# Kernel tuning notes

Hardware: AMD Instinct MI355X
Metric: run time of the kernel (lower is better)

Reference implementation:

```python
import jax, jax.numpy as jnp
import numpy as np

# Spike nonlinearity with straight-through surrogate gradient
# fwd: z = (v_scaled > 0); bwd: dz/dv = clamp(1 - |v_scaled|, min=0)
@jax.custom_vjp
def spike(v_scaled):
    return (v_scaled > 0).astype(v_scaled.dtype)

def _spike_fwd(v_scaled):
    return spike(v_scaled), v_scaled

def _spike_bwd(v_scaled, g):
    return (g * jnp.maximum(1.0 - jnp.abs(v_scaled), 0.0),)

spike.defvjp(_spike_fwd, _spike_bwd)

_H = np.array([-0.00285825, 0.09859432, 0.07954306, 0.08560576, 0.0910411, 0.10557652,
               0.04608637, 0.07096123, 0.01989892, 0.03412642, 0.03321506, 0.01300904,
               -0.02348068, 0.06102338, -0.00509757, 0.00051896], dtype=np.float32)
_D = np.array([0.04908372, -0.00948576, 0.00083943, 0.07961489, 0.08128168, 0.02395899,
               0.05197346, 0.01595683, 0.02185501, 0.01893722, 0.0074682, -0.00088913,
               0.01660369, 0.00298292, 0.0071363, 0.00279426], dtype=np.float32)
_T = np.array([0.20153396, -0.01304637, -0.19541621, 0.19903184, 0.1529713, -0.00479887,
               0.07102165, 0.02109929, 0.01368383, -0.00360851, -0.01454873, -0.03991705,
               -0.00440092, -0.06122432, -0.02989412, -0.04975629], dtype=np.float32)


def setup_inputs() -> dict:
    key = jax.random.key(0)
    x = jax.random.normal(key, (64, 1024, 1024), dtype=jnp.float32)
    return {
        "x": x,
        "h": jnp.asarray(_H),
        "d": jnp.asarray(_D),
        "T": jnp.asarray(_T),
    }


def reference(x, h, d, T):
    signs = jax.lax.stop_gradient(jnp.sign(x))  # detached in original
    x_abs = jnp.abs(x)

    def step(carry, hdT):
        v, z, out = carry
        ht, dt, Tt = hdT
        v = v - z * ht
        v_scaled = (v - Tt) / (jnp.abs(v) + 1.0)
        z = spike(v_scaled)
        out = out + z * dt
        return (v, z, out), None

    init = (x_abs, jnp.zeros_like(x_abs), jnp.zeros_like(x_abs))
    (_, _, out), _ = jax.lax.scan(step, init, (h, d, T))  # K=16 steps
    return out * signs
```

## Files before the change

kernel.cpp:

```cpp
#include <hip/hip_runtime.h>


#define BIN_B0 0x3D800000u
#define BIN_B1 0x3FC00000u
#define BIN_RANGE 0x02400000u
#define NBIN 4096
#define BIN_STEP 9216u
#define NSIDE_MAX 512
#define SCANTAG 0xFFC00000u

#define W_NSIDE 0
#define W_LO 1
#define W_HI 2
#define W_LUT 4
#define W_SIDE (W_LUT + NBIN)
#define WS_WORDS (W_SIDE + 4 * NSIDE_MAX)

__device__ __forceinline__ int predmask16(float a, const float* __restrict__ hh,
                                          const float* __restrict__ TT) {
    float v = a, z = 0.0f;
    int m = 0;
#pragma unroll
    for (int k = 0; k < 16; ++k) {
        v = fmaf(-z, hh[k], v);
        int zb = (v > TT[k]) ? 1 : 0;
        z = zb ? 1.0f : 0.0f;
        m |= zb << k;
    }
    return m;
}

__device__ __forceinline__ unsigned int valbits(int m, const float* __restrict__ dd) {
    float acc = 0.0f;
#pragma unroll
    for (int k = 0; k < 16; ++k)
        acc = ((m >> k) & 1) ? (acc + dd[k]) : acc;
    return __float_as_uint(acc);
}

__device__ __forceinline__ float scan_exact(unsigned int ab, const float* __restrict__ hh,
                                            const float* __restrict__ dd,
                                            const float* __restrict__ TT) {
    float v = __uint_as_float(ab), z = 0.0f, acc = 0.0f;
#pragma unroll
    for (int k = 0; k < 16; ++k) {
        v = fmaf(-z, hh[k], v);
        z = (v > TT[k]) ? 1.0f : 0.0f;
        acc = fmaf(z, dd[k], acc);
    }
    return acc;
}

__global__ __launch_bounds__(256) void snn_build(
    const float* __restrict__ h, const float* __restrict__ d,
    const float* __restrict__ T, unsigned int* __restrict__ ws) {
    const int u = blockIdx.x * 256 + threadIdx.x;
    if (u >= NBIN + 2) return;
    float hh[16], dd[16], TT[16];
#pragma unroll
    for (int k = 0; k < 16; ++k) { hh[k] = h[k]; dd[k] = d[k]; TT[k] = T[k]; }

    if (u == NBIN) {
        int mA = predmask16(__uint_as_float(0u), hh, TT);
        int mB = predmask16(__uint_as_float(BIN_B0 - 1u), hh, TT);
        ws[W_LO] = (mA == mB) ? valbits(mA, dd) : SCANTAG;
        return;
    }
    if (u == NBIN + 1) {
        int mA = predmask16(__uint_as_float(BIN_B1), hh, TT);
        int mB = predmask16(__uint_as_float(0x7F7FFFFFu), hh, TT);
        ws[W_HI] = (mA == mB) ? valbits(mA, dd) : SCANTAG;
        return;
    }

    const unsigned int Lb = BIN_B0 + (unsigned int)u * BIN_STEP;
    const unsigned int Hb = Lb + (BIN_STEP - 1u);
    const int mL = predmask16(__uint_as_float(Lb), hh, TT);
    const int mH = predmask16(__uint_as_float(Hb), hh, TT);
    if (mL == mH) { ws[W_LUT + u] = valbits(mL, dd); return; }

    unsigned int lo = Lb, hi = Hb;
    int mhi = mH;
    while (hi - lo > 1u) {
        unsigned int mid = lo + ((hi - lo) >> 1);
        int mm = predmask16(__uint_as_float(mid), hh, TT);
        if (mm == mL) lo = mid; else { hi = mid; mhi = mm; }
    }
    const unsigned int p1 = hi;
    const int m1 = mhi;

    unsigned int p2 = 0u;
    int m2 = m1;
    bool two = false, ok = true;
    if (m1 != mH) {
        lo = p1; hi = Hb; mhi = mH;
        while (hi - lo > 1u) {
            unsigned int mid = lo + ((hi - lo) >> 1);
            int mm = predmask16(__uint_as_float(mid), hh, TT);
            if (mm == m1) lo = mid; else { hi = mid; mhi = mm; }
        }
        p2 = hi;
        m2 = mhi;
        two = true;
        ok = (m2 == mH);
    }
    if (ok) {
        int idx = atomicAdd((int*)&ws[W_NSIDE], 1);
        if (idx < NSIDE_MAX) {
            const unsigned int o1 = p1 - Lb;
            const unsigned int o2 = two ? (p2 - Lb) : 0xFFFFu;
            ws[W_SIDE + 4 * idx + 0] = (o2 << 16) | o1;
            ws[W_SIDE + 4 * idx + 1] = valbits(mL, dd);
            ws[W_SIDE + 4 * idx + 2] = valbits(m1, dd);
            ws[W_SIDE + 4 * idx + 3] = valbits(m2, dd);
            ws[W_LUT + u] = 0x7F800000u | (unsigned int)idx;
        } else {
            ws[W_LUT + u] = SCANTAG;
        }
    } else {
        ws[W_LUT + u] = SCANTAG;
    }
}

__device__ __forceinline__ float lut_elem(float xe,
                                          const unsigned int* __restrict__ lutS,
                                          const uint4* __restrict__ sideS,
                                          unsigned int lo_e, unsigned int hi_e,
                                          const float* __restrict__ hh,
                                          const float* __restrict__ dd,
                                          const float* __restrict__ TT) {
    const unsigned int u = __float_as_uint(xe);
    const unsigned int sb = u & 0x80000000u;
    const unsigned int ab = u & 0x7FFFFFFFu;
    unsigned int t = ab - BIN_B0;
    t = (t > BIN_RANGE - 1u) ? (BIN_RANGE - 1u) : t;
    const unsigned int bin = ((t >> 10) * 58255u) >> 19;
    unsigned int eb = lutS[bin];
    eb = (ab < BIN_B0) ? lo_e : eb;
    eb = (ab >= BIN_B1) ? hi_e : eb;
    if (__builtin_expect((eb & 0x7F800000u) == 0x7F800000u, 0)) {
        if (eb != SCANTAG) {
            const uint4 e = sideS[eb & 0x3FFu];
            const unsigned int off = ab - (BIN_B0 + bin * BIN_STEP);
            const unsigned int o1 = e.x & 0xFFFFu;
            const unsigned int o2 = e.x >> 16;
            const unsigned int j = (off >= o1 ? 1u : 0u) + (off >= o2 ? 1u : 0u);
            unsigned int v = (j == 0u) ? e.y : ((j == 1u) ? e.z : e.w);
            eb = v;
        } else {
            eb = __float_as_uint(scan_exact(ab, hh, dd, TT));
        }
    }
    const float r = __uint_as_float(eb ^ sb);
    return (xe == 0.0f) ? 0.0f : r;
}

__global__ __launch_bounds__(256) void snn_apply(
    const float* __restrict__ x, const float* __restrict__ h,
    const float* __restrict__ d, const float* __restrict__ T,
    float* __restrict__ out, const unsigned int* __restrict__ ws,
    int n8, int n4, int n) {
    __shared__ unsigned int lutS[NBIN];
    __shared__ uint4 sideS[NSIDE_MAX];
    const int tid = threadIdx.x;

    float hh[16], dd[16], TT[16];
#pragma unroll
    for (int k = 0; k < 16; ++k) { hh[k] = h[k]; dd[k] = d[k]; TT[k] = T[k]; }

    for (int i = tid; i < NBIN; i += 256) lutS[i] = ws[W_LUT + i];
    const uint4* wside = reinterpret_cast<const uint4*>(ws + W_SIDE);
    for (int i = tid; i < NSIDE_MAX; i += 256) sideS[i] = wside[i];
    const unsigned int lo_e = ws[W_LO];
    const unsigned int hi_e = ws[W_HI];
    __syncthreads();

    const float4* __restrict__ x4 = reinterpret_cast<const float4*>(x);
    float4* __restrict__ o4 = reinterpret_cast<float4*>(out);
    const int gtid = blockIdx.x * blockDim.x + tid;
    const int nt = gridDim.x * blockDim.x;

#define APPLY4(vv)                                                             \
    {                                                                          \
        float4 ov;                                                             \
        ov.x = lut_elem(vv.x, lutS, sideS, lo_e, hi_e, hh, dd, TT);            \
        ov.y = lut_elem(vv.y, lutS, sideS, lo_e, hi_e, hh, dd, TT);            \
        ov.z = lut_elem(vv.z, lutS, sideS, lo_e, hi_e, hh, dd, TT);            \
        ov.w = lut_elem(vv.w, lutS, sideS, lo_e, hi_e, hh, dd, TT);            \
        vv = ov;                                                               \
    }

    int i = gtid;
    if (i < n8) {
        float4 ca = x4[2 * i], cb = x4[2 * i + 1];
        int nx = i + nt;
        while (nx < n8) {
            float4 pa = x4[2 * nx], pb = x4[2 * nx + 1];
            APPLY4(ca); APPLY4(cb);
            o4[2 * i] = ca; o4[2 * i + 1] = cb;
            ca = pa; cb = pb;
            i = nx; nx += nt;
        }
        APPLY4(ca); APPLY4(cb);
        o4[2 * i] = ca; o4[2 * i + 1] = cb;
    }
    for (int j = n8 * 2 + gtid; j < n4; j += nt) {
        float4 v = x4[j];
        APPLY4(v);
        o4[j] = v;
    }
    for (int j = n4 * 4 + gtid; j < n; j += nt)
        out[j] = lut_elem(x[j], lutS, sideS, lo_e, hi_e, hh, dd, TT);
#undef APPLY4
}

__global__ __launch_bounds__(256) void snn_direct(
    const float* __restrict__ x, const float* __restrict__ h,
    const float* __restrict__ d, const float* __restrict__ T,
    float* __restrict__ out, int n4, int n) {
    float hh[16], dd[16], TT[16];
#pragma unroll
    for (int k = 0; k < 16; ++k) { hh[k] = h[k]; dd[k] = d[k]; TT[k] = T[k]; }
    const float4* __restrict__ x4 = reinterpret_cast<const float4*>(x);
    float4* __restrict__ o4 = reinterpret_cast<float4*>(out);
    const int gtid = blockIdx.x * blockDim.x + threadIdx.x;
    const int nt = gridDim.x * blockDim.x;
    for (int i = gtid; i < n4; i += nt) {
        float4 v = x4[i], ov;
        float* pi = &v.x;
        float* po = &ov.x;
#pragma unroll
        for (int e = 0; e < 4; ++e) {
            float xe = pi[e];
            float acc = scan_exact(__float_as_uint(xe) & 0x7FFFFFFFu, hh, dd, TT);
            unsigned int rb =
                __float_as_uint(acc) ^ (__float_as_uint(xe) & 0x80000000u);
            po[e] = (xe == 0.0f) ? 0.0f : __uint_as_float(rb);
        }
        o4[i] = ov;
    }
    for (int j = n4 * 4 + gtid; j < n; j += nt) {
        float xe = x[j];
        float acc = scan_exact(__float_as_uint(xe) & 0x7FFFFFFFu, hh, dd, TT);
        unsigned int rb = __float_as_uint(acc) ^ (__float_as_uint(xe) & 0x80000000u);
        out[j] = (xe == 0.0f) ? 0.0f : __uint_as_float(rb);
    }
}

extern "C" void kernel_launch(void* const* d_in, const int* in_sizes, int n_in,
                              void* d_out, int out_size, void* d_ws, size_t ws_size,
                              hipStream_t stream) {
    const float* x = (const float*)d_in[0];
    const float* h = (const float*)d_in[1];
    const float* d = (const float*)d_in[2];
    const float* T = (const float*)d_in[3];
    float* out = (float*)d_out;

    const int n = in_sizes[0];
    const int n4 = n / 4;
    const int n8 = n / 8;

    if (ws_size < (size_t)WS_WORDS * 4) {
        int grid = 2048;
        const int needed = (n4 + 255) / 256;
        if (grid > needed) grid = needed > 0 ? needed : 1;
        snn_direct<<<grid, 256, 0, stream>>>(x, h, d, T, out, n4, n);
        return;
    }

    unsigned int* ws = (unsigned int*)d_ws;
    hipMemsetAsync(ws + W_NSIDE, 0, 4, stream);

    snn_build<<<(NBIN + 2 + 255) / 256, 256, 0, stream>>>(h, d, T, ws);

    int grid = 1536;
    const int needed = (n8 + 255) / 256;
    if (grid > needed) grid = needed > 0 ? needed : 1;
    snn_apply<<<grid, 256, 0, stream>>>(x, h, d, T, out, ws, n8, n4, n);
}
```

Before: 142.4 us.

## Generalize LUT breakpoints to variable count and drop per-element scan fallback

The build kernel now records up to 12 breakpoints per bin in a packed shared array instead of at most two in a fixed side table. The apply kernel resolves mixed bins with a short linear search over those breakpoints and no longer keeps the 48 h/d/T registers or the inline exact-scan fallback. A global flag moves any unrepresentable case to a separate whole-kernel exact-scan path. The memset is replaced by a tiny init kernel. This is meant to reduce register pressure and divergence in the hot loop, at the cost of a data-dependent loop and a larger shared-memory footprint.

```diff
diff --git a/kernel.cpp b/kernel.cpp
--- a/kernel.cpp
+++ b/kernel.cpp
@@ -5,16 +5,16 @@
 #define BIN_B1 0x3FC00000u
 #define BIN_RANGE 0x02400000u
 #define NBIN 4096
-#define BIN_STEP 9216u
-#define NSIDE_MAX 512
-#define SCANTAG 0xFFC00000u
-
-#define W_NSIDE 0
-#define W_LO 1
-#define W_HI 2
+#define CMAX 12
+#define BP_CAP 2048
+
+#define W_CNT 0
+#define W_FLAG 1
+#define W_LO 2
+#define W_HI 3
 #define W_LUT 4
-#define W_SIDE (W_LUT + NBIN)
-#define WS_WORDS (W_SIDE + 4 * NSIDE_MAX)
+#define W_BP (W_LUT + NBIN)
+#define WS_WORDS (W_BP + BP_CAP)
 
 __device__ __forceinline__ int predmask16(float a, const float* __restrict__ hh,
                                           const float* __restrict__ TT) {
@@ -49,6 +49,10 @@
         acc = fmaf(z, dd[k], acc);
     }
     return acc;
+}
+
+__global__ void snn_init(unsigned int* __restrict__ ws) {
+    if (threadIdx.x == 0) { ws[W_CNT] = 0u; ws[W_FLAG] = 0u; }
 }
 
 __global__ __launch_bounds__(256) void snn_build(
@@ -63,72 +67,60 @@
     if (u == NBIN) {
         int mA = predmask16(__uint_as_float(0u), hh, TT);
         int mB = predmask16(__uint_as_float(BIN_B0 - 1u), hh, TT);
-        ws[W_LO] = (mA == mB) ? valbits(mA, dd) : SCANTAG;
+        if (mA == mB) ws[W_LO] = valbits(mA, dd);
+        else { ws[W_LO] = 0u; atomicOr(&ws[W_FLAG], 1u); }
         return;
     }
     if (u == NBIN + 1) {
         int mA = predmask16(__uint_as_float(BIN_B1), hh, TT);
         int mB = predmask16(__uint_as_float(0x7F7FFFFFu), hh, TT);
-        ws[W_HI] = (mA == mB) ? valbits(mA, dd) : SCANTAG;
+        if (mA == mB) ws[W_HI] = valbits(mA, dd);
+        else { ws[W_HI] = 0u; atomicOr(&ws[W_FLAG], 1u); }
         return;
     }
 
-    const unsigned int Lb = BIN_B0 + (unsigned int)u * BIN_STEP;
-    const unsigned int Hb = Lb + (BIN_STEP - 1u);
+    const unsigned int Lb = BIN_B0 + (unsigned int)u * 9216u;
+    const unsigned int Hb = Lb + 9215u;
     const int mL = predmask16(__uint_as_float(Lb), hh, TT);
     const int mH = predmask16(__uint_as_float(Hb), hh, TT);
     if (mL == mH) { ws[W_LUT + u] = valbits(mL, dd); return; }
 
-    unsigned int lo = Lb, hi = Hb;
-    int mhi = mH;
-    while (hi - lo > 1u) {
-        unsigned int mid = lo + ((hi - lo) >> 1);
-        int mm = predmask16(__uint_as_float(mid), hh, TT);
-        if (mm == mL) lo = mid; else { hi = mid; mhi = mm; }
-    }
-    const unsigned int p1 = hi;
-    const int m1 = mhi;
-
-    unsigned int p2 = 0u;
-    int m2 = m1;
-    bool two = false, ok = true;
-    if (m1 != mH) {
-        lo = p1; hi = Hb; mhi = mH;
+    unsigned int bp[CMAX];
+    int vm[CMAX + 1];
+    vm[0] = mL;
+    int cnt = 0, cur = mL;
+    unsigned int anchor = Lb;
+    bool bad = false;
+    while (cur != mH) {
+        if (cnt == CMAX) { bad = true; break; }
+        unsigned int lo = anchor, hi = Hb;
+        int mhi = mH;
         while (hi - lo > 1u) {
             unsigned int mid = lo + ((hi - lo) >> 1);
             int mm = predmask16(__uint_as_float(mid), hh, TT);
-            if (mm == m1) lo = mid; else { hi = mid; mhi = mm; }
-        }
-        p2 = hi;
-        m2 = mhi;
-        two = true;
-        ok = (m2 == mH);
-    }
-    if (ok) {
-        int idx = atomicAdd((int*)&ws[W_NSIDE], 1);
-        if (idx < NSIDE_MAX) {
-            const unsigned int o1 = p1 - Lb;
-            const unsigned int o2 = two ? (p2 - Lb) : 0xFFFFu;
-            ws[W_SIDE + 4 * idx + 0] = (o2 << 16) | o1;
-            ws[W_SIDE + 4 * idx + 1] = valbits(mL, dd);
-            ws[W_SIDE + 4 * idx + 2] = valbits(m1, dd);
-            ws[W_SIDE + 4 * idx + 3] = valbits(m2, dd);
-            ws[W_LUT + u] = 0x7F800000u | (unsigned int)idx;
-        } else {
-            ws[W_LUT + u] = SCANTAG;
-        }
-    } else {
-        ws[W_LUT + u] = SCANTAG;
-    }
+            if (mm == cur) lo = mid; else { hi = mid; mhi = mm; }
+        }
+        bp[cnt] = hi;
+        vm[cnt + 1] = mhi;
+        ++cnt;
+        cur = mhi;
+        anchor = hi;
+    }
+    if (bad) { atomicOr(&ws[W_FLAG], 1u); ws[W_LUT + u] = 0u; return; }
+
+    const unsigned int need = 2u * (unsigned int)cnt + 1u;
+    const unsigned int start = atomicAdd(&ws[W_CNT], need);
+    if (start + need > BP_CAP) { atomicOr(&ws[W_FLAG], 1u); ws[W_LUT + u] = 0u; return; }
+    for (int k = 0; k < cnt; ++k) ws[W_BP + start + k] = bp[k];
+    for (int j = 0; j <= cnt; ++j)
+        ws[W_BP + start + cnt + j] = valbits(vm[j], dd);
+    ws[W_LUT + u] = 0x7F800000u | ((unsigned int)cnt << 19) | start;
 }
 
 __device__ __forceinline__ float lut_elem(float xe,
                                           const unsigned int* __restrict__ lutS,
-                                          const uint4* __restrict__ sideS,
-                                          unsigned int lo_e, unsigned int hi_e,
-                                          const float* __restrict__ hh,
-                                          const float* __restrict__ dd,
-                                          const float* __restrict__ TT) {
+                                          const unsigned int* __restrict__ bpS,
+                                          unsigned int lo_e, unsigned int hi_e) {
     const unsigned int u = __float_as_uint(xe);
     const unsigned int sb = u & 0x80000000u;
     const unsigned int ab = u & 0x7FFFFFFFu;
@@ -138,18 +130,13 @@
     unsigned int eb = lutS[bin];
     eb = (ab < BIN_B0) ? lo_e : eb;
     eb = (ab >= BIN_B1) ? hi_e : eb;
-    if (__builtin_expect((eb & 0x7F800000u) == 0x7F800000u, 0)) {
-        if (eb != SCANTAG) {
-            const uint4 e = sideS[eb & 0x3FFu];
-            const unsigned int off = ab - (BIN_B0 + bin * BIN_STEP);
-            const unsigned int o1 = e.x & 0xFFFFu;
-            const unsigned int o2 = e.x >> 16;
-            const unsigned int j = (off >= o1 ? 1u : 0u) + (off >= o2 ? 1u : 0u);
-            unsigned int v = (j == 0u) ? e.y : ((j == 1u) ? e.z : e.w);
-            eb = v;
-        } else {
-            eb = __float_as_uint(scan_exact(ab, hh, dd, TT));
-        }
+    if ((eb & 0x7F800000u) == 0x7F800000u) {
+        const unsigned int s = eb & 0x7FFFFu;
+        const unsigned int c = (eb >> 19) & 0xFu;
+        unsigned int j = 0;
+        for (unsigned int k = 0; k < c; ++k)
+            j += (ab >= bpS[s + k]) ? 1u : 0u;
+        eb = bpS[s + c + j];
     }
     const float r = __uint_as_float(eb ^ sb);
     return (xe == 0.0f) ? 0.0f : r;
@@ -161,16 +148,12 @@
     float* __restrict__ out, const unsigned int* __restrict__ ws,
     int n8, int n4, int n) {
     __shared__ unsigned int lutS[NBIN];
-    __shared__ uint4 sideS[NSIDE_MAX];
+    __shared__ unsigned int bpS[BP_CAP];
     const int tid = threadIdx.x;
 
-    float hh[16], dd[16], TT[16];
-#pragma unroll
-    for (int k = 0; k < 16; ++k) { hh[k] = h[k]; dd[k] = d[k]; TT[k] = T[k]; }
-
     for (int i = tid; i < NBIN; i += 256) lutS[i] = ws[W_LUT + i];
-    const uint4* wside = reinterpret_cast<const uint4*>(ws + W_SIDE);
-    for (int i = tid; i < NSIDE_MAX; i += 256) sideS[i] = wside[i];
+    for (int i = tid; i < BP_CAP; i += 256) bpS[i] = ws[W_BP + i];
+    const unsigned int flag = ws[W_FLAG];
     const unsigned int lo_e = ws[W_LO];
     const unsigned int hi_e = ws[W_HI];
     __syncthreads();
@@ -180,38 +163,63 @@
     const int gtid = blockIdx.x * blockDim.x + tid;
     const int nt = gridDim.x * blockDim.x;
 
+    if (flag == 0u) {
 #define APPLY4(vv)                                                             \
-    {                                                                          \
-        float4 ov;                                                             \
-        ov.x = lut_elem(vv.x, lutS, sideS, lo_e, hi_e, hh, dd, TT);            \
-        ov.y = lut_elem(vv.y, lutS, sideS, lo_e, hi_e, hh, dd, TT);            \
-        ov.z = lut_elem(vv.z, lutS, sideS, lo_e, hi_e, hh, dd, TT);            \
-        ov.w = lut_elem(vv.w, lutS, sideS, lo_e, hi_e, hh, dd, TT);            \
-        vv = ov;                                                               \
-    }
-
-    int i = gtid;
-    if (i < n8) {
-        float4 ca = x4[2 * i], cb = x4[2 * i + 1];
-        int nx = i + nt;
-        while (nx < n8) {
-            float4 pa = x4[2 * nx], pb = x4[2 * nx + 1];
+        {                                                                      \
+            float4 ov;                                                         \
+            ov.x = lut_elem(vv.x, lutS, bpS, lo_e, hi_e);                      \
+            ov.y = lut_elem(vv.y, lutS, bpS, lo_e, hi_e);                      \
+            ov.z = lut_elem(vv.z, lutS, bpS, lo_e, hi_e);                      \
+            ov.w = lut_elem(vv.w, lutS, bpS, lo_e, hi_e);                      \
+            vv = ov;                                                           \
+        }
+        int i = gtid;
+        if (i < n8) {
+            float4 ca = x4[2 * i], cb = x4[2 * i + 1];
+            int nx = i + nt;
+            while (nx < n8) {
+                float4 pa = x4[2 * nx], pb = x4[2 * nx + 1];
+                APPLY4(ca); APPLY4(cb);
+                o4[2 * i] = ca; o4[2 * i + 1] = cb;
+                ca = pa; cb = pb;
+                i = nx; nx += nt;
+            }
             APPLY4(ca); APPLY4(cb);
             o4[2 * i] = ca; o4[2 * i + 1] = cb;
-            ca = pa; cb = pb;
-            i = nx; nx += nt;
-        }
-        APPLY4(ca); APPLY4(cb);
-        o4[2 * i] = ca; o4[2 * i + 1] = cb;
-    }
-    for (int j = n8 * 2 + gtid; j < n4; j += nt) {
-        float4 v = x4[j];
-        APPLY4(v);
-        o4[j] = v;
-    }
-    for (int j = n4 * 4 + gtid; j < n; j += nt)
-        out[j] = lut_elem(x[j], lutS, sideS, lo_e, hi_e, hh, dd, TT);
+        }
+        for (int j = n8 * 2 + gtid; j < n4; j += nt) {
+            float4 v = x4[j];
+            APPLY4(v);
+            o4[j] = v;
+        }
+        for (int j = n4 * 4 + gtid; j < n; j += nt)
+            out[j] = lut_elem(x[j], lutS, bpS, lo_e, hi_e);
 #undef APPLY4
+    } else {
+        float hh[16], dd[16], TT[16];
+#pragma unroll
+        for (int k = 0; k < 16; ++k) { hh[k] = h[k]; dd[k] = d[k]; TT[k] = T[k]; }
+        for (int j = gtid; j < n4; j += nt) {
+            float4 v = x4[j], ov;
+            float* pi = &v.x;
+            float* po = &ov.x;
+#pragma unroll
+            for (int e = 0; e < 4; ++e) {
+                float xe = pi[e];
+                float acc = scan_exact(__float_as_uint(xe) & 0x7FFFFFFFu, hh, dd, TT);
+                unsigned int rb =
+                    __float_as_uint(acc) ^ (__float_as_uint(xe) & 0x80000000u);
+                po[e] = (xe == 0.0f) ? 0.0f : __uint_as_float(rb);
+            }
+            o4[j] = ov;
+        }
+        for (int j = n4 * 4 + gtid; j < n; j += nt) {
+            float xe = x[j];
+            float acc = scan_exact(__float_as_uint(xe) & 0x7FFFFFFFu, hh, dd, TT);
+            unsigned int rb = __float_as_uint(acc) ^ (__float_as_uint(xe) & 0x80000000u);
+            out[j] = (xe == 0.0f) ? 0.0f : __uint_as_float(rb);
+        }
+    }
 }
 
 __global__ __launch_bounds__(256) void snn_direct(
@@ -269,8 +277,7 @@
     }
 
     unsigned int* ws = (unsigned int*)d_ws;
-    hipMemsetAsync(ws + W_NSIDE, 0, 4, stream);
-
+    snn_init<<<1, 64, 0, stream>>>(ws);
     snn_build<<<(NBIN + 2 + 255) / 256, 256, 0, stream>>>(h, d, T, ws);
 
     int grid = 1536;
```

After: 143.7 us. About the same (+0.9%).
